# Performance work log

Measured on AMD Instinct MI355X. Metric: run time of the kernel, lower is better.

The kernel has to match this reference:

```python
import math
import jax, jax.numpy as jnp
import numpy as np

D, NH, NL, NP = 256, 8, 4, 4
C = D // NH
VALUE_SHAPES = np.array([[128, 128], [64, 64], [32, 32], [16, 16]], dtype=np.int32)


def _offset_bias():
    # Faithful to MSDeformAttn._reset_parameters grid init for sampling_offsets.bias
    th = np.arange(NH, dtype=np.float32) * (2.0 * np.pi / NH)
    g = np.stack([np.cos(th), np.sin(th)], -1)                      # [NH,2]
    g = g / np.abs(g).max(-1, keepdims=True)
    g = np.tile(g[:, None, None, :], (1, NL, NP, 1))                # [NH,NL,NP,2]
    g = g * np.arange(1, NP + 1, dtype=np.float32)[None, None, :, None]
    return jnp.asarray(g.reshape(-1), jnp.float32)


def setup_inputs() -> dict:
    key = jax.random.key(0)
    ks = jax.random.split(key, 10)
    bs, Q = 8, 2048
    LV = int((VALUE_SHAPES[:, 0] * VALUE_SHAPES[:, 1]).sum())
    s = 0.02
    return {
        "query": jax.random.normal(ks[0], (bs, Q, D), jnp.float32),
        "refer_bbox": jax.random.uniform(ks[1], (bs, Q, NL, 2), jnp.float32),
        "value": jax.random.normal(ks[2], (bs, LV, D), jnp.float32),
        "value_shapes": VALUE_SHAPES,  # static numpy (shapes must be compile-time constants)
        "W_value": jax.random.normal(ks[3], (D, D), jnp.float32) * s,
        "b_value": jnp.zeros((D,), jnp.float32),
        "W_off": jax.random.normal(ks[4], (D, NH * NL * NP * 2), jnp.float32) * 0.01,
        "b_off": _offset_bias(),
        "W_attn": jax.random.normal(ks[5], (D, NH * NL * NP), jnp.float32) * s,
        "b_attn": jnp.zeros((NH * NL * NP,), jnp.float32),
        "W_out": jax.random.normal(ks[6], (D, D), jnp.float32) * s,
        "b_out": jnp.zeros((D,), jnp.float32),
    }


def _ms_deform_attn(value, shapes, loc, attn):
    # value: [bs,LV,NH,C], loc: [bs,Q,NH,NL,NP,2] in [0,1], attn: [bs,Q,NH,NL,NP]
    bs, LV = value.shape[:2]
    Q = loc.shape[1]
    BH = bs * NH
    v = value.transpose(0, 2, 1, 3).reshape(BH, LV, C)              # [BH,LV,C]
    loc = loc.transpose(0, 2, 1, 3, 4, 5).reshape(BH, Q, NL, NP, 2)
    attn = attn.transpose(0, 2, 1, 3, 4).reshape(BH, Q, NL, NP)
    acc = jnp.zeros((BH, Q, C), value.dtype)
    start = 0
    for lvl in range(NL):
        H, W = int(shapes[lvl, 0]), int(shapes[lvl, 1])
        img = v[:, start:start + H * W]                             # [BH,HW,C]
        start += H * W
        # grid_sample(align_corners=False): pixel coord = loc * size - 0.5
        x = loc[:, :, lvl, :, 0] * W - 0.5                          # [BH,Q,NP]
        y = loc[:, :, lvl, :, 1] * H - 0.5
        x0 = jnp.floor(x); y0 = jnp.floor(y)
        fx = x - x0; fy = y - y0
        x0i = x0.astype(jnp.int32); y0i = y0.astype(jnp.int32)
        samp = jnp.zeros((BH, Q, NP, C), value.dtype)
        for dx, dy in ((0, 0), (1, 0), (0, 1), (1, 1)):
            xi = x0i + dx; yi = y0i + dy
            valid = (xi >= 0) & (xi < W) & (yi >= 0) & (yi < H)     # zero padding
            w = (fx if dx else 1.0 - fx) * (fy if dy else 1.0 - fy)
            w = jnp.where(valid, w, 0.0)
            idx = jnp.clip(yi, 0, H - 1) * W + jnp.clip(xi, 0, W - 1)
            g = jnp.take_along_axis(img, idx.reshape(BH, Q * NP)[..., None], axis=1)
            samp = samp + w[..., None] * g.reshape(BH, Q, NP, C)
        acc = acc + (samp * attn[:, :, lvl, :, None]).sum(2)
    return acc.reshape(bs, NH, Q, C).transpose(0, 2, 1, 3).reshape(bs, Q, D)


def reference(query, refer_bbox, value, value_shapes, W_value, b_value,
              W_off, b_off, W_attn, b_attn, W_out, b_out):
    shapes = np.asarray(value_shapes)  # static
    bs, Q = query.shape[:2]
    LV = value.shape[1]
    v = (value @ W_value + b_value).reshape(bs, LV, NH, C)
    off = (query @ W_off + b_off).reshape(bs, Q, NH, NL, NP, 2)
    attn = jax.nn.softmax((query @ W_attn + b_attn).reshape(bs, Q, NH, NL * NP), -1)
    attn = attn.reshape(bs, Q, NH, NL, NP)
    norm = jnp.asarray(shapes[:, ::-1], query.dtype)                # (W,H) per level
    loc = refer_bbox[:, :, None, :, None, :] + off / norm[None, None, None, :, None, :]
    out = _ms_deform_attn(v, shapes, loc, attn)
    return out @ W_out + b_out
```

## Files before the change

### kernel.cpp

```cpp
#include <hip/hip_runtime.h>
#include <hip/hip_bf16.h>

#define D_MODEL 256
#define NHEAD   8
#define NLVL    4
#define NPTS    4
#define CH      32
#define QTOT    2048
#define BS      8
#define LVTOT   21760
#define KDIM    256

typedef __attribute__((ext_vector_type(8))) short bf16x8;
typedef __attribute__((ext_vector_type(4))) float f32x4;

__device__ inline float bf_lo(unsigned u) { unsigned t = u << 16; float f; __builtin_memcpy(&f, &t, 4); return f; }
__device__ inline float bf_hi(unsigned u) { unsigned t = u & 0xffff0000u; float f; __builtin_memcpy(&f, &t, 4); return f; }
__device__ inline float bfu2f(unsigned short s) { unsigned t = (unsigned)s << 16; float f; __builtin_memcpy(&f, &t, 4); return f; }
__device__ inline unsigned short f2bfu(float f) { __hip_bfloat16 h = __float2bfloat16(f); unsigned short u; __builtin_memcpy(&u, &h, 2); return u; }

__global__ __launch_bounds__(256)
void convert_W(const float* __restrict__ W, __hip_bfloat16* __restrict__ Wt, int sh) {
    int t = blockIdx.x * 256 + threadIdx.x;
    int k = t >> sh, n = t & ((1 << sh) - 1);
    Wt[n * 256 + k] = __float2bfloat16(W[(k << sh) + n]);
}

__global__ __launch_bounds__(256)
void convert_q(const float* __restrict__ q, __hip_bfloat16* __restrict__ qb) {
    int t = blockIdx.x * 256 + threadIdx.x;
    float4 f = ((const float4*)q)[t];
    __hip_bfloat16 h4[4] = {__float2bfloat16(f.x), __float2bfloat16(f.y),
                            __float2bfloat16(f.z), __float2bfloat16(f.w)};
    ((uint2*)qb)[t] = *(const uint2*)h4;
}

#define LDV 136
#define LDP 72

__global__ __launch_bounds__(256, 2)
void gemm_value_mfma(const float* __restrict__ A,
                     const __hip_bfloat16* __restrict__ Wt,
                     const float* __restrict__ bias,
                     __hip_bfloat16* __restrict__ v) {
    __shared__ __align__(16) char smem[2 * 128 * LDV * 2];
    __hip_bfloat16* As = (__hip_bfloat16*)smem;
    __hip_bfloat16* Bs = (__hip_bfloat16*)(smem + 128 * LDV * 2);
    __hip_bfloat16* Cs = (__hip_bfloat16*)smem;

    const int tid  = threadIdx.x;
    const int lane = tid & 63;
    const int wave = tid >> 6;
    const int wr   = wave >> 1;
    const int wc   = wave & 1;
    const int cb      = blockIdx.x * 128;
    const int rowBase = blockIdx.y * 128;

    const int m0   = lane & 15;
    const int quad = lane >> 4;

    f32x4 acc[4][4] = {};

    for (int kc = 0; kc < KDIM; kc += 128) {
#pragma unroll
        for (int it = 0; it < 16; ++it) {
            const int row = it * 8 + (tid >> 5);
            float4 f = *(const float4*)(A + (size_t)(rowBase + row) * KDIM + kc + (tid & 31) * 4);
            __hip_bfloat16 t4[4] = {__float2bfloat16(f.x), __float2bfloat16(f.y),
                                    __float2bfloat16(f.z), __float2bfloat16(f.w)};
            *(uint2*)&As[row * LDV + (tid & 31) * 4] = *(const uint2*)t4;
        }
#pragma unroll
        for (int it = 0; it < 8; ++it) {
            const int row = it * 16 + (tid >> 4);
            uint4 u = *(const uint4*)(Wt + (size_t)(cb + row) * KDIM + kc + (tid & 15) * 8);
            *(uint4*)&Bs[row * LDV + (tid & 15) * 8] = u;
        }
        __syncthreads();

#pragma unroll
        for (int ks = 0; ks < 4; ++ks) {
            bf16x8 af[4], bfv[4];
#pragma unroll
            for (int i = 0; i < 4; ++i)
                af[i] = *(const bf16x8*)&As[(wr * 64 + i * 16 + m0) * LDV + ks * 32 + quad * 8];
#pragma unroll
            for (int j = 0; j < 4; ++j)
                bfv[j] = *(const bf16x8*)&Bs[(wc * 64 + j * 16 + m0) * LDV + ks * 32 + quad * 8];
#pragma unroll
            for (int i = 0; i < 4; ++i)
#pragma unroll
                for (int j = 0; j < 4; ++j)
                    acc[i][j] = __builtin_amdgcn_mfma_f32_16x16x32_bf16(af[i], bfv[j], acc[i][j], 0, 0, 0);
        }
        __syncthreads();
    }

    const int b = rowBase / LVTOT;
    const int pixBase = rowBase - b * LVTOT;
#pragma unroll
    for (int half = 0; half < 2; ++half) {
        if (wr == half) {
#pragma unroll
            for (int j = 0; j < 4; ++j) {
                const int lcol = wc * 64 + j * 16 + m0;
                const float bv = bias[cb + lcol];
#pragma unroll
                for (int i = 0; i < 4; ++i) {
                    const int lrow = i * 16 + quad * 4;
#pragma unroll
                    for (int r = 0; r < 4; ++r)
                        Cs[(lrow + r) * LDV + lcol] = __float2bfloat16(acc[i][j][r] + bv);
                }
            }
        }
        __syncthreads();
        char* dst = (char*)v + (size_t)(b * LVTOT + pixBase + half * 64) * 512 + cb * 2;
        const char* src = (const char*)Cs;
#pragma unroll
        for (int itr = 0; itr < 4; ++itr) {
            const int o = itr * 4096 + tid * 16;
            const int row = o >> 8;
            const int c   = o & 255;
            uint4 val = *(const uint4*)(src + row * (LDV * 2) + c);
            *(uint4*)(dst + (size_t)row * 512 + c) = val;
        }
        if (half == 0) __syncthreads();
    }
}

struct StorePlain {
    float* o;
    int ncol;
    const float* bias;
    __device__ void operator()(int row, int col, float val) const {
        o[(size_t)row * ncol + col] = val + bias[col];
    }
};

struct StoreSplit {
    float* o1;
    float* o2;
    const float* b1;
    const float* b2;
    __device__ void operator()(int row, int col, float val) const {
        if (col < 256) o1[(size_t)row * 256 + col] = val + b1[col];
        else           o2[(size_t)row * 128 + (col - 256)] = val + b2[col - 256];
    }
};

template <typename Store>
__global__ __launch_bounds__(256, 4)
void gemm_bf16_small(const __hip_bfloat16* __restrict__ A,
                     const __hip_bfloat16* __restrict__ Wt, Store store) {
    __shared__ __align__(16) __hip_bfloat16 As[64 * LDP];
    __shared__ __align__(16) __hip_bfloat16 Bs[128 * LDP];

    const int tid  = threadIdx.x;
    const int lane = tid & 63;
    const int wave = tid >> 6;
    const int wr   = wave >> 1;
    const int wc   = wave & 1;
    const int rowBase = blockIdx.x * 64;
    const int cb      = blockIdx.y * 128;

    const int m0   = lane & 15;
    const int quad = lane >> 4;

    const int sr = tid >> 3;
    const int sc = tid & 7;

    f32x4 acc[2][4] = {};

    for (int kc = 0; kc < KDIM; kc += 64) {
#pragma unroll
        for (int it = 0; it < 2; ++it) {
            const int row = it * 32 + sr;
            uint4 ua = *(const uint4*)(A + (size_t)(rowBase + row) * KDIM + kc + sc * 8);
            *(uint4*)&As[row * LDP + sc * 8] = ua;
        }
#pragma unroll
        for (int it = 0; it < 4; ++it) {
            const int row = it * 32 + sr;
            uint4 ub = *(const uint4*)(Wt + (size_t)(cb + row) * KDIM + kc + sc * 8);
            *(uint4*)&Bs[row * LDP + sc * 8] = ub;
        }
        __syncthreads();

#pragma unroll
        for (int ks = 0; ks < 2; ++ks) {
            bf16x8 af[2], bfv[4];
#pragma unroll
            for (int i = 0; i < 2; ++i)
                af[i] = *(const bf16x8*)&As[(wr * 32 + i * 16 + m0) * LDP + ks * 32 + quad * 8];
#pragma unroll
            for (int j = 0; j < 4; ++j)
                bfv[j] = *(const bf16x8*)&Bs[(wc * 64 + j * 16 + m0) * LDP + ks * 32 + quad * 8];
#pragma unroll
            for (int i = 0; i < 2; ++i)
#pragma unroll
                for (int j = 0; j < 4; ++j)
                    acc[i][j] = __builtin_amdgcn_mfma_f32_16x16x32_bf16(af[i], bfv[j], acc[i][j], 0, 0, 0);
        }
        __syncthreads();
    }

#pragma unroll
    for (int j = 0; j < 4; ++j) {
        const int col = cb + wc * 64 + j * 16 + m0;
#pragma unroll
        for (int i = 0; i < 2; ++i) {
            const int row0 = rowBase + wr * 32 + i * 16 + quad * 4;
#pragma unroll
            for (int r = 0; r < 4; ++r)
                store(row0 + r, col, acc[i][j][r]);
        }
    }
}

__global__ __launch_bounds__(256)
void sample_kernel(const float* __restrict__ off_ws,
                   const float* __restrict__ logits_ws,
                   const float* __restrict__ bbox,
                   const __hip_bfloat16* __restrict__ v,
                   __hip_bfloat16* __restrict__ acc_bf) {
    __shared__ __align__(16) float off_s[8 * 256];
    __shared__ __align__(16) float attn_s[8 * 128];
    __shared__ float bbox_s[64];
    __shared__ __align__(16) int idx_s[1024 * 4];
    __shared__ __align__(8) unsigned short w_s[1024 * 4];

    const int tid = threadIdx.x;
    const int b = blockIdx.x & 7;
    const int gq0 = b * QTOT + (blockIdx.x >> 3) * 8;

    const float4* osrc = (const float4*)(off_ws + (size_t)gq0 * 256);
    ((float4*)off_s)[tid] = osrc[tid];
    ((float4*)off_s)[tid + 256] = osrc[tid + 256];
    const float4* lsrc = (const float4*)(logits_ws + (size_t)gq0 * 128);
    ((float4*)attn_s)[tid] = lsrc[tid];
    if (tid < 64) bbox_s[tid] = bbox[(size_t)gq0 * 8 + tid];
    __syncthreads();

    if (tid < 64) {
        int qq = tid >> 3, h = tid & 7;
        float* p = attn_s + qq * 128 + h * 16;
        float m = p[0];
#pragma unroll
        for (int i = 1; i < 16; ++i) m = fmaxf(m, p[i]);
        float e[16], s = 0.f;
#pragma unroll
        for (int i = 0; i < 16; ++i) { e[i] = __expf(p[i] - m); s += e[i]; }
        float inv = 1.f / s;
#pragma unroll
        for (int i = 0; i < 16; ++i) p[i] = e[i] * inv;
    }
    __syncthreads();

#pragma unroll
    for (int r = 0; r < 4; ++r) {
        const int tap = tid + r * 256;
        const int qq = tap >> 7, h = (tap >> 4) & 7, l = (tap >> 2) & 3, p = tap & 3;
        const int Wd = 128 >> l;
        const int st = (l == 0) ? 0 : (l == 1) ? 16384 : (l == 2) ? 20480 : 21504;

        const float bx = bbox_s[qq * 8 + l * 2 + 0];
        const float by = bbox_s[qq * 8 + l * 2 + 1];
        const float ox = off_s[qq * 256 + h * 32 + l * 8 + p * 2 + 0];
        const float oy = off_s[qq * 256 + h * 32 + l * 8 + p * 2 + 1];
        const float att = attn_s[qq * 128 + h * 16 + l * 4 + p];

        const float x = bx * (float)Wd + ox - 0.5f;
        const float y = by * (float)Wd + oy - 0.5f;
        const float x0f = floorf(x), y0f = floorf(y);
        const float fx = x - x0f, fy = y - y0f;
        const int x0 = (int)x0f, y0 = (int)y0f;
        const int x1 = x0 + 1, y1 = y0 + 1;
        const bool vx0 = (unsigned)x0 < (unsigned)Wd;
        const bool vx1 = (unsigned)x1 < (unsigned)Wd;
        const bool vy0 = (unsigned)y0 < (unsigned)Wd;
        const bool vy1 = (unsigned)y1 < (unsigned)Wd;
        const int cx0 = min(max(x0, 0), Wd - 1), cx1 = min(max(x1, 0), Wd - 1);
        const int cy0 = min(max(y0, 0), Wd - 1), cy1 = min(max(y1, 0), Wd - 1);

        int4 idx;
        idx.x = (st + cy0 * Wd + cx0) << 9;
        idx.y = (st + cy0 * Wd + cx1) << 9;
        idx.z = (st + cy1 * Wd + cx0) << 9;
        idx.w = (st + cy1 * Wd + cx1) << 9;
        float w0 = (vx0 && vy0) ? (1.f - fx) * (1.f - fy) * att : 0.f;
        float w1 = (vx1 && vy0) ? fx * (1.f - fy) * att : 0.f;
        float w2 = (vx0 && vy1) ? (1.f - fx) * fy * att : 0.f;
        float w3 = (vx1 && vy1) ? fx * fy * att : 0.f;

        *(int4*)&idx_s[tap * 4] = idx;
        unsigned short w4[4] = {f2bfu(w0), f2bfu(w1), f2bfu(w2), f2bfu(w3)};
        *(uint2*)&w_s[tap * 4] = *(const uint2*)w4;
    }
    __syncthreads();

    const int lane = tid & 63;
    const int wave = tid >> 6;
    const int g = lane >> 4;
    const int c2 = lane & 15;

    const char* vbase = (const char*)v + (size_t)b * LVTOT * 512 + c2 * 4;

    for (int i = 0; i < 16; ++i) {
        const int pair = wave * 16 + i;
        const int qq = pair >> 3, hh = pair & 7;
        const char* slab = vbase + hh * 64;
        const int tbase = qq * 128 + hh * 16;

        float ax0 = 0.f, ay0 = 0.f, ax1 = 0.f, ay1 = 0.f, ax2 = 0.f, ay2 = 0.f, ax3 = 0.f, ay3 = 0.f;
#pragma unroll
        for (int ts = 0; ts < 4; ++ts) {
            const int tap = tbase + ts * 4 + g;
            const int4 idx = *(const int4*)&idx_s[tap * 4];
            const ushort4 ww = *(const ushort4*)&w_s[tap * 4];
            unsigned u0 = *(const unsigned*)(slab + idx.x);
            unsigned u1 = *(const unsigned*)(slab + idx.y);
            unsigned u2 = *(const unsigned*)(slab + idx.z);
            unsigned u3 = *(const unsigned*)(slab + idx.w);
            float w0 = bfu2f(ww.x), w1 = bfu2f(ww.y), w2 = bfu2f(ww.z), w3 = bfu2f(ww.w);
            ax0 += w0 * bf_lo(u0); ay0 += w0 * bf_hi(u0);
            ax1 += w1 * bf_lo(u1); ay1 += w1 * bf_hi(u1);
            ax2 += w2 * bf_lo(u2); ay2 += w2 * bf_hi(u2);
            ax3 += w3 * bf_lo(u3); ay3 += w3 * bf_hi(u3);
        }
        float sx = (ax0 + ax1) + (ax2 + ax3);
        float sy = (ay0 + ay1) + (ay2 + ay3);
        sx += __shfl_xor(sx, 16); sy += __shfl_xor(sy, 16);
        sx += __shfl_xor(sx, 32); sy += __shfl_xor(sy, 32);
        if (g == 0) {
            __hip_bfloat16 h2[2] = {__float2bfloat16(sx), __float2bfloat16(sy)};
            unsigned packed; __builtin_memcpy(&packed, h2, 4);
            *(unsigned*)((char*)acc_bf + ((size_t)(gq0 + qq) * 256 + hh * 32 + c2 * 2) * 2) = packed;
        }
    }
}

extern "C" void kernel_launch(void* const* d_in, const int* in_sizes, int n_in,
                              void* d_out, int out_size, void* d_ws, size_t ws_size,
                              hipStream_t stream) {
    const float* query   = (const float*)d_in[0];
    const float* bbox    = (const float*)d_in[1];
    const float* value   = (const float*)d_in[2];
    const float* W_value = (const float*)d_in[4];
    const float* b_value = (const float*)d_in[5];
    const float* W_off   = (const float*)d_in[6];
    const float* b_off   = (const float*)d_in[7];
    const float* W_attn  = (const float*)d_in[8];
    const float* b_attn  = (const float*)d_in[9];
    const float* W_out   = (const float*)d_in[10];
    const float* b_out   = (const float*)d_in[11];
    float* out = (float*)d_out;

    char* ws = (char*)d_ws;
    __hip_bfloat16* v_ws  = (__hip_bfloat16*)ws;
    float* off_ws         = (float*)(ws + 89128960);
    float* logits_ws      = (float*)(ws + 89128960 + 16777216);
    __hip_bfloat16* acc_bf = (__hip_bfloat16*)(ws + 89128960 + 16777216 + 8388608);
    __hip_bfloat16* q_bf   = (__hip_bfloat16*)(ws + 89128960 + 16777216 + 8388608 + 8388608);

    __hip_bfloat16* Wt_v    = acc_bf;
    __hip_bfloat16* Wt_off  = acc_bf + 65536;
    __hip_bfloat16* Wt_attn = acc_bf + 131072;
    __hip_bfloat16* Wt_out  = q_bf;

    const int NQ = BS * QTOT;
    const int NVROWS = BS * LVTOT;

    convert_q<<<NQ * KDIM / 1024, 256, 0, stream>>>(query, q_bf);
    convert_W<<<256, 256, 0, stream>>>(W_value, Wt_v, 8);
    convert_W<<<256, 256, 0, stream>>>(W_off, Wt_off, 8);
    convert_W<<<128, 256, 0, stream>>>(W_attn, Wt_attn, 7);

    gemm_value_mfma<<<dim3(2, NVROWS / 128), 256, 0, stream>>>(value, Wt_v, b_value, v_ws);

    gemm_bf16_small<<<dim3(NQ / 64, 3), 256, 0, stream>>>(
        q_bf, Wt_off, StoreSplit{off_ws, logits_ws, b_off, b_attn});

    convert_W<<<256, 256, 0, stream>>>(W_out, Wt_out, 8);

    sample_kernel<<<NQ / 8, 256, 0, stream>>>(off_ws, logits_ws, bbox, v_ws, acc_bf);

    gemm_bf16_small<<<dim3(NQ / 64, 2), 256, 0, stream>>>(
        acc_bf, Wt_out, StorePlain{out, 256, b_out});
}
```

Baseline: 411.3 us.

## Double-buffer value GEMM shared tiles with register prefetch over BK=64 steps

```diff
diff --git a/kernel.cpp b/kernel.cpp
--- a/kernel.cpp
+++ b/kernel.cpp
@@ -35,18 +35,18 @@
     ((uint2*)qb)[t] = *(const uint2*)h4;
 }
 
-#define LDV 136
+#define BK  64
 #define LDP 72
+#define LDE 136
 
 __global__ __launch_bounds__(256, 2)
 void gemm_value_mfma(const float* __restrict__ A,
                      const __hip_bfloat16* __restrict__ Wt,
                      const float* __restrict__ bias,
                      __hip_bfloat16* __restrict__ v) {
-    __shared__ __align__(16) char smem[2 * 128 * LDV * 2];
-    __hip_bfloat16* As = (__hip_bfloat16*)smem;
-    __hip_bfloat16* Bs = (__hip_bfloat16*)(smem + 128 * LDV * 2);
-    __hip_bfloat16* Cs = (__hip_bfloat16*)smem;
+    __shared__ __align__(16) __hip_bfloat16 As[2][128 * LDP];
+    __shared__ __align__(16) __hip_bfloat16 Bs[2][128 * LDP];
+    __hip_bfloat16* Cs = &As[0][0];
 
     const int tid  = threadIdx.x;
     const int lane = tid & 63;
@@ -59,41 +59,69 @@
     const int m0   = lane & 15;
     const int quad = lane >> 4;
 
+    const int ar = tid >> 4;
+    const int ac = tid & 15;
+    const int br = tid >> 3;
+    const int bc = tid & 7;
+
     f32x4 acc[4][4] = {};
 
-    for (int kc = 0; kc < KDIM; kc += 128) {
-#pragma unroll
-        for (int it = 0; it < 16; ++it) {
-            const int row = it * 8 + (tid >> 5);
-            float4 f = *(const float4*)(A + (size_t)(rowBase + row) * KDIM + kc + (tid & 31) * 4);
-            __hip_bfloat16 t4[4] = {__float2bfloat16(f.x), __float2bfloat16(f.y),
-                                    __float2bfloat16(f.z), __float2bfloat16(f.w)};
-            *(uint2*)&As[row * LDV + (tid & 31) * 4] = *(const uint2*)t4;
-        }
-#pragma unroll
-        for (int it = 0; it < 8; ++it) {
-            const int row = it * 16 + (tid >> 4);
-            uint4 u = *(const uint4*)(Wt + (size_t)(cb + row) * KDIM + kc + (tid & 15) * 8);
-            *(uint4*)&Bs[row * LDV + (tid & 15) * 8] = u;
-        }
-        __syncthreads();
-
-#pragma unroll
-        for (int ks = 0; ks < 4; ++ks) {
+    auto ldA = [&](int i, int kc) {
+        return *(const float4*)(A + (size_t)(rowBase + i * 16 + ar) * KDIM + kc + ac * 4);
+    };
+    auto ldB = [&](int i, int kc) {
+        return *(const uint4*)(Wt + (size_t)(cb + i * 32 + br) * KDIM + kc + bc * 8);
+    };
+    auto stA = [&](int buf, int i, float4 f) {
+        __hip_bfloat16 t4[4] = {__float2bfloat16(f.x), __float2bfloat16(f.y),
+                                __float2bfloat16(f.z), __float2bfloat16(f.w)};
+        *(uint2*)&As[buf][(i * 16 + ar) * LDP + ac * 4] = *(const uint2*)t4;
+    };
+    auto stB = [&](int buf, int i, uint4 u) {
+        *(uint4*)&Bs[buf][(i * 32 + br) * LDP + bc * 8] = u;
+    };
+
+    float4 a0, a1, a2, a3, a4, a5, a6, a7;
+    uint4  b0, b1, b2, b3;
+
+    a0 = ldA(0, 0); a1 = ldA(1, 0); a2 = ldA(2, 0); a3 = ldA(3, 0);
+    a4 = ldA(4, 0); a5 = ldA(5, 0); a6 = ldA(6, 0); a7 = ldA(7, 0);
+    b0 = ldB(0, 0); b1 = ldB(1, 0); b2 = ldB(2, 0); b3 = ldB(3, 0);
+    stA(0, 0, a0); stA(0, 1, a1); stA(0, 2, a2); stA(0, 3, a3);
+    stA(0, 4, a4); stA(0, 5, a5); stA(0, 6, a6); stA(0, 7, a7);
+    stB(0, 0, b0); stB(0, 1, b1); stB(0, 2, b2); stB(0, 3, b3);
+    __syncthreads();
+
+#pragma unroll
+    for (int t = 0; t < 4; ++t) {
+        const int cur = t & 1, nxt = cur ^ 1;
+        if (t < 3) {
+            const int kc = (t + 1) * BK;
+            a0 = ldA(0, kc); a1 = ldA(1, kc); a2 = ldA(2, kc); a3 = ldA(3, kc);
+            a4 = ldA(4, kc); a5 = ldA(5, kc); a6 = ldA(6, kc); a7 = ldA(7, kc);
+            b0 = ldB(0, kc); b1 = ldB(1, kc); b2 = ldB(2, kc); b3 = ldB(3, kc);
+        }
+#pragma unroll
+        for (int ks = 0; ks < 2; ++ks) {
             bf16x8 af[4], bfv[4];
 #pragma unroll
             for (int i = 0; i < 4; ++i)
-                af[i] = *(const bf16x8*)&As[(wr * 64 + i * 16 + m0) * LDV + ks * 32 + quad * 8];
+                af[i] = *(const bf16x8*)&As[cur][(wr * 64 + i * 16 + m0) * LDP + ks * 32 + quad * 8];
 #pragma unroll
             for (int j = 0; j < 4; ++j)
-                bfv[j] = *(const bf16x8*)&Bs[(wc * 64 + j * 16 + m0) * LDV + ks * 32 + quad * 8];
+                bfv[j] = *(const bf16x8*)&Bs[cur][(wc * 64 + j * 16 + m0) * LDP + ks * 32 + quad * 8];
 #pragma unroll
             for (int i = 0; i < 4; ++i)
 #pragma unroll
                 for (int j = 0; j < 4; ++j)
                     acc[i][j] = __builtin_amdgcn_mfma_f32_16x16x32_bf16(af[i], bfv[j], acc[i][j], 0, 0, 0);
         }
-        __syncthreads();
+        if (t < 3) {
+            stA(nxt, 0, a0); stA(nxt, 1, a1); stA(nxt, 2, a2); stA(nxt, 3, a3);
+            stA(nxt, 4, a4); stA(nxt, 5, a5); stA(nxt, 6, a6); stA(nxt, 7, a7);
+            stB(nxt, 0, b0); stB(nxt, 1, b1); stB(nxt, 2, b2); stB(nxt, 3, b3);
+            __syncthreads();
+        }
     }
 
     const int b = rowBase / LVTOT;
@@ -110,7 +138,7 @@
                     const int lrow = i * 16 + quad * 4;
 #pragma unroll
                     for (int r = 0; r < 4; ++r)
-                        Cs[(lrow + r) * LDV + lcol] = __float2bfloat16(acc[i][j][r] + bv);
+                        Cs[(lrow + r) * LDE + lcol] = __float2bfloat16(acc[i][j][r] + bv);
                 }
             }
         }
@@ -122,7 +150,7 @@
             const int o = itr * 4096 + tid * 16;
             const int row = o >> 8;
             const int c   = o & 255;
-            uint4 val = *(const uint4*)(src + row * (LDV * 2) + c);
+            uint4 val = *(const uint4*)(src + row * (LDE * 2) + c);
             *(uint4*)(dst + (size_t)row * 512 + c) = val;
         }
         if (half == 0) __syncthreads();
```

Result: no change. 417.4 us (+1.5%).
